# Performance work log

Hardware: AMD Instinct MI355X
Metric: run time of the kernel (lower is better)

## Reference

```python
import jax, jax.numpy as jnp
import numpy as np

B, N, C, K, H, W = 2, 16, 256, 64, 64, 64
NUM_HEADS = 8


def setup_inputs() -> dict:
    key = jax.random.key(0)
    ks = jax.random.split(key, 7)
    return {
        "value": jax.random.normal(ks[0], (B, N, C, H, W), dtype=jnp.float32),
        "key_map": jax.random.normal(ks[1], (B, K, H, W), dtype=jnp.float32),
        "state": jax.random.normal(ks[2], (B, N, K, C), dtype=jnp.float32),
        "b_w": jax.random.normal(ks[3], (NUM_HEADS, C), dtype=jnp.float32) * 0.06,
        "a_w": jax.random.normal(ks[4], (NUM_HEADS, C), dtype=jnp.float32) * 0.06,
        "A_log": jax.random.normal(ks[5], (NUM_HEADS,), dtype=jnp.float32),
        "dt_bias": jax.random.normal(ks[6], (NUM_HEADS,), dtype=jnp.float32),
    }


def reference(value, key_map, state, b_w, a_w, A_log, dt_bias):
    # Gated delta-rule erase-write memory update (state != None branch).
    num_heads = b_w.shape[0]
    rep = value.shape[2] // num_heads  # value_dim // num_heads

    # softmax over key channel dim (stable; matches max-subtract + softmax)
    key_n = jax.nn.softmax(key_map, axis=1)  # [B,K,H,W]

    # v_k = einsum('bkhw, bjhw,bnjv -> bnkv'): fuse via key gram matrix
    # (avoids materializing v_old [B,N,C,H,W])
    gram = jnp.einsum('bkhw,bjhw->bkj', key_n, key_n)      # [B,K,K]
    v_k = jnp.einsum('bkj,bnjv->bnkv', gram, state)        # [B,N,K,C]

    # erase gate beta: sigmoid(state @ b_proj^T), repeat over head groups
    beta = jax.nn.sigmoid(jnp.einsum('bnkc,hc->bnkh', state, b_w))
    beta = jnp.repeat(beta, rep, axis=3)                   # [B,N,K,C]

    # write term
    vk_t = jnp.einsum('bkhw,bnvhw->bnkv', key_n, value)    # [B,N,K,C]

    # decay gate alpha = -exp(A_log) * softplus(state @ a_proj^T + dt_bias)
    alpha = -jnp.exp(A_log) * jax.nn.softplus(
        jnp.einsum('bnkc,hc->bnkh', state, a_w) + dt_bias)
    alpha = jnp.repeat(alpha, rep, axis=3)                 # [B,N,K,C]

    new_state = alpha * (state - beta * v_k) + beta * vk_t  # [B,N,K,C]

    readout = jnp.einsum('bkhw,bnkv->bnvhw', key_n, new_state)  # [B,N,C,H,W]
    return readout
```

## Files before the change

kernel.cpp:

```cpp
#include <hip/hip_runtime.h>
#include <hip/hip_bf16.h>

#define BB 2
#define NN 16
#define CC 256
#define KK 64
#define HW 4096
#define NH 8

typedef __attribute__((ext_vector_type(4))) float f32x4;
typedef __attribute__((ext_vector_type(8))) short s16x8;
typedef __attribute__((ext_vector_type(4))) short s16x4;

__device__ __forceinline__ short f2bf(float f) {
    __hip_bfloat16 h = __float2bfloat16(f);
    return *reinterpret_cast<short*>(&h);
}
__device__ __forceinline__ float bf2f(short s) {
    unsigned int u = ((unsigned int)(unsigned short)s) << 16;
    float f; __builtin_memcpy(&f, &u, 4); return f;
}

__global__ __launch_bounds__(64) void k_softmax(const float* __restrict__ km,
                                                short* __restrict__ kbf,
                                                short* __restrict__ kbfT) {
    const int b = blockIdx.x >> 7;
    const int hw = (blockIdx.x & 127) * 32 + (threadIdx.x & 31);
    const int half = threadIdx.x >> 5;
    const float* p = km + ((size_t)b * KK + half * 32) * HW + hw;
    float x[32];
    float m = -1e30f;
#pragma unroll
    for (int k = 0; k < 32; k++) { x[k] = p[(size_t)k * HW]; m = fmaxf(m, x[k]); }
    m = fmaxf(m, __shfl_xor(m, 32, 64));
    float s = 0.f;
#pragma unroll
    for (int k = 0; k < 32; k++) { x[k] = __expf(x[k] - m); s += x[k]; }
    s += __shfl_xor(s, 32, 64);
    const float inv = 1.f / s;
    short* q2 = kbf + ((size_t)b * KK + half * 32) * HW + hw;
#pragma unroll
    for (int k = 0; k < 32; k++) {
        x[k] *= inv;
        q2[(size_t)k * HW] = f2bf(x[k]);
    }
    short* q3 = kbfT + ((size_t)b * HW + hw) * KK + half * 32;
#pragma unroll
    for (int k8 = 0; k8 < 32; k8 += 8) {
        s16x8 v;
#pragma unroll
        for (int j = 0; j < 8; j++) v[j] = f2bf(x[k8 + j]);
        *(s16x8*)(q3 + k8) = v;
    }
}

__global__ __launch_bounds__(256) void k_gram(const short* __restrict__ kbf,
                                              float* __restrict__ gram) {
    const int tid = threadIdx.x;
    const int id = blockIdx.x;
    const int b = (id >= 2080) ? 1 : 0;
    const int t = id - b * 2080;
    int k = (int)((sqrtf(8.f * (float)t + 1.f) - 1.f) * 0.5f);
    while ((k + 1) * (k + 2) / 2 <= t) k++;
    while (k * (k + 1) / 2 > t) k--;
    const int j = t - k * (k + 1) / 2;

    const short* pa = kbf + ((size_t)b * KK + k) * HW + tid * 16;
    const short* pb = kbf + ((size_t)b * KK + j) * HW + tid * 16;
    const s16x8 a0 = *(const s16x8*)pa, a1 = *(const s16x8*)(pa + 8);
    const s16x8 b0 = *(const s16x8*)pb, b1 = *(const s16x8*)(pb + 8);
    float s = 0.f;
#pragma unroll
    for (int i = 0; i < 8; i++) {
        s = fmaf(bf2f(a0[i]), bf2f(b0[i]), s);
        s = fmaf(bf2f(a1[i]), bf2f(b1[i]), s);
    }
#pragma unroll
    for (int off = 32; off; off >>= 1) s += __shfl_down(s, off, 64);
    __shared__ float red[4];
    if ((tid & 63) == 0) red[tid >> 6] = s;
    __syncthreads();
    if (tid == 0) {
        const float tot = red[0] + red[1] + red[2] + red[3];
        gram[((size_t)b * KK + k) * KK + j] = tot;
        gram[((size_t)b * KK + j) * KK + k] = tot;
    }
}

__global__ __launch_bounds__(256) void k_gates(const float* __restrict__ state,
                                               const float* __restrict__ b_w,
                                               const float* __restrict__ a_w,
                                               const float* __restrict__ A_log,
                                               const float* __restrict__ dt_bias,
                                               float* __restrict__ betaH,
                                               float* __restrict__ alphaH) {
    const int tid = threadIdx.x;
    const int id = blockIdx.x;
    const int k = id & 63;
    const int bn = id >> 6;
    const float s = state[((size_t)bn * KK + k) * CC + tid];

    float pb[NH], pa[NH];
#pragma unroll
    for (int h = 0; h < NH; h++) {
        pb[h] = s * b_w[h * CC + tid];
        pa[h] = s * a_w[h * CC + tid];
    }
#pragma unroll
    for (int off = 32; off; off >>= 1) {
#pragma unroll
        for (int h = 0; h < NH; h++) {
            pb[h] += __shfl_down(pb[h], off, 64);
            pa[h] += __shfl_down(pa[h], off, 64);
        }
    }
    __shared__ float red[4][2 * NH];
    const int wave = tid >> 6, lane = tid & 63;
    if (lane == 0) {
#pragma unroll
        for (int h = 0; h < NH; h++) { red[wave][h] = pb[h]; red[wave][NH + h] = pa[h]; }
    }
    __syncthreads();
    const int h = tid >> 5;
    float braw = 0.f, araw = 0.f;
#pragma unroll
    for (int w = 0; w < 4; w++) { braw += red[w][h]; araw += red[w][NH + h]; }
    if ((tid & 31) == 0) {
        const float beta = 1.f / (1.f + __expf(-braw));
        const float xx = araw + dt_bias[h];
        const float sp = fmaxf(xx, 0.f) + log1pf(__expf(-fabsf(xx)));
        const float alpha = -__expf(A_log[h]) * sp;
        betaH[(size_t)id * NH + h] = beta;
        alphaH[(size_t)id * NH + h] = alpha;
    }
}

__global__ __launch_bounds__(512) void k_vkt_part(const short* __restrict__ kbf,
                                                  const float* __restrict__ value,
                                                  float* __restrict__ pbuf) {
    const int tid = threadIdx.x;
    const int id = blockIdx.x;
    const int hs = id & 7;
    const int bn = id >> 3;
    const int b  = bn >> 4;
    const int w = tid >> 6, lane = tid & 63;
    const int l15 = lane & 15, hi = lane >> 4;
    const int hw0 = hs * 512;

    __shared__ short Bs[2][256 * 64];
    __shared__ short As[2][64 * 64];

    const int sr = tid >> 3;
    const int sj = tid & 7;
    const float* vbase = value + (size_t)bn * CC * HW + hw0;
    const short* abase = kbf + ((size_t)b * KK + sr) * HW + hw0 + sj * 8;

    f32x4 stgB[2][4][2];
    s16x8 stgA[2];

#define LOADREG(set_, t_)                                                      \
    {                                                                          \
        _Pragma("unroll") for (int i = 0; i < 4; i++) {                        \
            const float* p_ = vbase + (size_t)(sr + i * 64) * HW               \
                              + (t_) * 64 + sj * 8;                            \
            stgB[set_][i][0] = *(const f32x4*)p_;                              \
            stgB[set_][i][1] = *(const f32x4*)(p_ + 4);                        \
        }                                                                      \
        stgA[set_] = *(const s16x8*)(abase + (t_) * 64);                       \
    }
#define WRITE_LDS(set_, buf_)                                                  \
    {                                                                          \
        _Pragma("unroll") for (int i = 0; i < 4; i++) {                        \
            const int r_ = sr + i * 64;                                        \
            s16x8 tv_;                                                         \
            _Pragma("unroll") for (int e = 0; e < 4; e++) {                    \
                tv_[e]     = f2bf(stgB[set_][i][0][e]);                        \
                tv_[4 + e] = f2bf(stgB[set_][i][1][e]);                        \
            }                                                                  \
            *(s16x8*)&Bs[buf_][r_ * 64 + ((sj ^ (r_ & 7)) * 8)] = tv_;         \
        }                                                                      \
        *(s16x8*)&As[buf_][sr * 64 + ((sj ^ (sr & 7)) * 8)] = stgA[set_];      \
    }

    f32x4 acc[4][2];
#pragma unroll
    for (int m = 0; m < 4; m++)
#pragma unroll
        for (int n = 0; n < 2; n++) acc[m][n] = (f32x4){0.f, 0.f, 0.f, 0.f};

    LOADREG(0, 0);
    LOADREG(1, 1);
    WRITE_LDS(0, 0);
    asm volatile("s_waitcnt lgkmcnt(0)" ::: "memory");
    __builtin_amdgcn_s_barrier();

#pragma unroll
    for (int t = 0; t < 8; t++) {
        const int buf = t & 1;
        if (t + 2 < 8) LOADREG(buf, t + 2);

        const int swz = l15 & 7;
#pragma unroll
        for (int s = 0; s < 2; s++) {
            s16x8 bfr[2];
#pragma unroll
            for (int n = 0; n < 2; n++)
                bfr[n] = *(const s16x8*)&Bs[buf][(w * 32 + n * 16 + l15) * 64 +
                                                (((s * 4 + hi) ^ swz) * 8)];
#pragma unroll
            for (int m = 0; m < 4; m++) {
                const s16x8 afr = *(const s16x8*)&As[buf][(m * 16 + l15) * 64 +
                                                          (((s * 4 + hi) ^ swz) * 8)];
                acc[m][0] = __builtin_amdgcn_mfma_f32_16x16x32_bf16(afr, bfr[0],
                                                                    acc[m][0], 0, 0, 0);
                acc[m][1] = __builtin_amdgcn_mfma_f32_16x16x32_bf16(afr, bfr[1],
                                                                    acc[m][1], 0, 0, 0);
            }
        }
        asm volatile("s_waitcnt lgkmcnt(0)" ::: "memory");
        __builtin_amdgcn_s_barrier();
        if (t + 1 < 8) {
            WRITE_LDS((t + 1) & 1, (t + 1) & 1);
            asm volatile("s_waitcnt lgkmcnt(0)" ::: "memory");
            __builtin_amdgcn_s_barrier();
        }
    }
#undef LOADREG
#undef WRITE_LDS

    float* op = pbuf + (size_t)id * (KK * CC);
#pragma unroll
    for (int m = 0; m < 4; m++)
#pragma unroll
        for (int n = 0; n < 2; n++)
#pragma unroll
            for (int r = 0; r < 4; r++)
                op[(m * 16 + hi * 4 + r) * CC + w * 32 + n * 16 + l15] = acc[m][n][r];
}

__global__ __launch_bounds__(256) void k_combine(const float* __restrict__ pbuf,
                                                 const float* __restrict__ gram,
                                                 const float* __restrict__ state,
                                                 const float* __restrict__ betaH,
                                                 const float* __restrict__ alphaH,
                                                 short* __restrict__ nsT) {
    const int tid = threadIdx.x;
    const int id = blockIdx.x;
    const int ct = id & 15;
    const int bn = id >> 4;
    const int b  = bn >> 4;
    const int head = ct >> 1;

    __shared__ float gramL[KK][65];
    __shared__ float stL[KK][17];
    __shared__ float alphaL[KK], betaL[KK];
    __shared__ float nsb[KK][17];

    for (int i = tid; i < KK * KK; i += 256)
        gramL[i >> 6][i & 63] = gram[(size_t)b * KK * KK + i];
    for (int i = tid; i < KK * 16; i += 256)
        stL[i >> 4][i & 15] = state[((size_t)bn * KK + (i >> 4)) * CC + ct * 16 + (i & 15)];
    if (tid < KK) {
        alphaL[tid] = alphaH[((size_t)bn * KK + tid) * NH + head];
        betaL[tid]  = betaH[((size_t)bn * KK + tid) * NH + head];
    }
    __syncthreads();

    const int k = tid >> 2, cq = (tid & 3) * 4;

    f32x4 vkt = (f32x4){0.f, 0.f, 0.f, 0.f};
#pragma unroll
    for (int hs = 0; hs < 8; hs++) {
        const f32x4 p = *(const f32x4*)(pbuf + ((size_t)(bn * 8 + hs) * KK + k) * CC +
                                        ct * 16 + cq);
        vkt += p;
    }

    float vk[4] = {0.f, 0.f, 0.f, 0.f};
#pragma unroll 8
    for (int j = 0; j < KK; j++) {
        const float g = gramL[k][j];
        vk[0] = fmaf(g, stL[j][cq + 0], vk[0]);
        vk[1] = fmaf(g, stL[j][cq + 1], vk[1]);
        vk[2] = fmaf(g, stL[j][cq + 2], vk[2]);
        vk[3] = fmaf(g, stL[j][cq + 3], vk[3]);
    }
    const float al = alphaL[k], be = betaL[k];
#pragma unroll
    for (int i = 0; i < 4; i++)
        nsb[k][cq + i] = al * (stL[k][cq + i] - be * vk[i]) + be * vkt[i];
    __syncthreads();

    const int c = tid >> 4, k4 = (tid & 15) * 4;
    s16x4 v;
#pragma unroll
    for (int i = 0; i < 4; i++) v[i] = f2bf(nsb[k4 + i][c]);
    *(s16x4*)(nsT + ((size_t)bn * CC + ct * 16 + c) * KK + k4) = v;
}

__global__ __launch_bounds__(256) void k_readout_mfma(const short* __restrict__ kbfT,
                                                      const short* __restrict__ nsT,
                                                      float* __restrict__ out) {
    const int tid = threadIdx.x;
    const int id = blockIdx.x;
    const int hwt = id & 63;
    const int bn  = id >> 6;
    const int b   = bn >> 4;
    const int w = tid >> 6, lane = tid & 63;
    const int l15 = lane & 15, hi = lane >> 4;
    const int hw0 = hwt * 64 + w * 16;

    const short* Bp = kbfT + ((size_t)b * HW + hw0 + l15) * KK + hi * 8;
    const s16x8 b0 = *(const s16x8*)Bp;
    const s16x8 b1 = *(const s16x8*)(Bp + 32);

    const short* Ap = nsT + ((size_t)bn * CC + l15) * KK + hi * 8;
    float* op = out + ((size_t)bn * CC + hi * 4) * HW + hw0 + l15;

#pragma unroll
    for (int ct = 0; ct < 16; ct++) {
        const s16x8 a0 = *(const s16x8*)(Ap + (size_t)(ct * 16) * KK);
        const s16x8 a1 = *(const s16x8*)(Ap + (size_t)(ct * 16) * KK + 32);
        f32x4 acc = (f32x4){0.f, 0.f, 0.f, 0.f};
        acc = __builtin_amdgcn_mfma_f32_16x16x32_bf16(a0, b0, acc, 0, 0, 0);
        acc = __builtin_amdgcn_mfma_f32_16x16x32_bf16(a1, b1, acc, 0, 0, 0);
#pragma unroll
        for (int r = 0; r < 4; r++)
            op[(size_t)(ct * 16 + r) * HW] = acc[r];
    }
}

extern "C" void kernel_launch(void* const* d_in, const int* in_sizes, int n_in,
                              void* d_out, int out_size, void* d_ws, size_t ws_size,
                              hipStream_t stream) {
    const float* value   = (const float*)d_in[0];
    const float* key_map = (const float*)d_in[1];
    const float* state   = (const float*)d_in[2];
    const float* b_w     = (const float*)d_in[3];
    const float* a_w     = (const float*)d_in[4];
    const float* A_log   = (const float*)d_in[5];
    const float* dt_bias = (const float*)d_in[6];
    float* out = (float*)d_out;

    short* kbf   = (short*)d_ws;
    short* kbfT  = kbf + 524288;
    float* gram  = (float*)(kbfT + 524288);
    float* betaH = gram + 8192;
    float* alphaH= betaH + 16384;
    short* nsT   = (short*)(alphaH + 16384);
    float* pbuf  = (float*)(nsT + 524288);

    k_softmax<<<BB * (HW / 32), 64, 0, stream>>>(key_map, kbf, kbfT);
    k_gram<<<BB * (KK * (KK + 1) / 2), 256, 0, stream>>>(kbf, gram);
    k_gates<<<BB * NN * KK, 256, 0, stream>>>(state, b_w, a_w, A_log, dt_bias,
                                              betaH, alphaH);
    k_vkt_part<<<BB * NN * 8, 512, 0, stream>>>(kbf, value, pbuf);
    k_combine<<<BB * NN * 16, 256, 0, stream>>>(pbuf, gram, state, betaH, alphaH, nsT);
    k_readout_mfma<<<BB * NN * (HW / 64), 256, 0, stream>>>(kbfT, nsT, out);
}
```

Before: 103.5 us.

## Merge softmax and gate kernels; swap MFMA operands for vectorized stores

```diff
diff --git a/kernel.cpp b/kernel.cpp
--- a/kernel.cpp
+++ b/kernel.cpp
@@ -21,36 +21,89 @@
     float f; __builtin_memcpy(&f, &u, 4); return f;
 }
 
-__global__ __launch_bounds__(64) void k_softmax(const float* __restrict__ km,
-                                                short* __restrict__ kbf,
-                                                short* __restrict__ kbfT) {
-    const int b = blockIdx.x >> 7;
-    const int hw = (blockIdx.x & 127) * 32 + (threadIdx.x & 31);
-    const int half = threadIdx.x >> 5;
-    const float* p = km + ((size_t)b * KK + half * 32) * HW + hw;
-    float x[32];
-    float m = -1e30f;
-#pragma unroll
-    for (int k = 0; k < 32; k++) { x[k] = p[(size_t)k * HW]; m = fmaxf(m, x[k]); }
-    m = fmaxf(m, __shfl_xor(m, 32, 64));
-    float s = 0.f;
-#pragma unroll
-    for (int k = 0; k < 32; k++) { x[k] = __expf(x[k] - m); s += x[k]; }
-    s += __shfl_xor(s, 32, 64);
-    const float inv = 1.f / s;
-    short* q2 = kbf + ((size_t)b * KK + half * 32) * HW + hw;
-#pragma unroll
-    for (int k = 0; k < 32; k++) {
-        x[k] *= inv;
-        q2[(size_t)k * HW] = f2bf(x[k]);
-    }
-    short* q3 = kbfT + ((size_t)b * HW + hw) * KK + half * 32;
-#pragma unroll
-    for (int k8 = 0; k8 < 32; k8 += 8) {
-        s16x8 v;
-#pragma unroll
-        for (int j = 0; j < 8; j++) v[j] = f2bf(x[k8 + j]);
-        *(s16x8*)(q3 + k8) = v;
+__global__ __launch_bounds__(256) void k_pre(const float* __restrict__ state,
+                                             const float* __restrict__ b_w,
+                                             const float* __restrict__ a_w,
+                                             const float* __restrict__ A_log,
+                                             const float* __restrict__ dt_bias,
+                                             float* __restrict__ betaH,
+                                             float* __restrict__ alphaH,
+                                             const float* __restrict__ km,
+                                             short* __restrict__ kbf,
+                                             short* __restrict__ kbfT) {
+    __shared__ float red[4][2 * NH];
+    const int tid = threadIdx.x;
+    const int bid = blockIdx.x;
+
+    if (bid < BB * NN * KK) {
+        const int id = bid;
+        const int bn = id >> 6;
+        const int k = id & 63;
+        const float s = state[((size_t)bn * KK + k) * CC + tid];
+
+        float pb[NH], pa[NH];
+#pragma unroll
+        for (int h = 0; h < NH; h++) {
+            pb[h] = s * b_w[h * CC + tid];
+            pa[h] = s * a_w[h * CC + tid];
+        }
+#pragma unroll
+        for (int off = 32; off; off >>= 1) {
+#pragma unroll
+            for (int h = 0; h < NH; h++) {
+                pb[h] += __shfl_down(pb[h], off, 64);
+                pa[h] += __shfl_down(pa[h], off, 64);
+            }
+        }
+        const int wave = tid >> 6, lane = tid & 63;
+        if (lane == 0) {
+#pragma unroll
+            for (int h = 0; h < NH; h++) { red[wave][h] = pb[h]; red[wave][NH + h] = pa[h]; }
+        }
+        __syncthreads();
+        const int h = tid >> 5;
+        float braw = 0.f, araw = 0.f;
+#pragma unroll
+        for (int w = 0; w < 4; w++) { braw += red[w][h]; araw += red[w][NH + h]; }
+        if ((tid & 31) == 0) {
+            const float beta = 1.f / (1.f + __expf(-braw));
+            const float xx = araw + dt_bias[h];
+            const float sp = fmaxf(xx, 0.f) + log1pf(__expf(-fabsf(xx)));
+            const float alpha = -__expf(A_log[h]) * sp;
+            betaH[(size_t)id * NH + h] = beta;
+            alphaH[(size_t)id * NH + h] = alpha;
+        }
+    } else {
+        const int sid = bid - BB * NN * KK;
+        const int b = sid >> 5;
+        const int w = tid >> 6, lane = tid & 63;
+        const int hw = (sid & 31) * 128 + w * 32 + (lane & 31);
+        const int half = lane >> 5;
+        const float* p = km + ((size_t)b * KK + half * 32) * HW + hw;
+        float x[32];
+        float m = -1e30f;
+#pragma unroll
+        for (int k = 0; k < 32; k++) { x[k] = p[(size_t)k * HW]; m = fmaxf(m, x[k]); }
+        m = fmaxf(m, __shfl_xor(m, 32, 64));
+        float s = 0.f;
+#pragma unroll
+        for (int k = 0; k < 32; k++) { x[k] = __expf(x[k] - m); s += x[k]; }
+        s += __shfl_xor(s, 32, 64);
+        const float inv = 1.f / s;
+        short* q2 = kbf + ((size_t)b * KK + half * 32) * HW + hw;
+#pragma unroll
+        for (int k = 0; k < 32; k++) {
+            x[k] *= inv;
+            q2[(size_t)k * HW] = f2bf(x[k]);
+        }
+        short* q3 = kbfT + ((size_t)b * HW + hw) * KK + half * 32;
+#pragma unroll
+        for (int k8 = 0; k8 < 32; k8 += 8) {
+            s16x8 v;
+#pragma unroll
+            for (int j = 0; j < 8; j++) v[j] = f2bf(x[k8 + j]);
+            *(s16x8*)(q3 + k8) = v;
+        }
     }
 }
 
@@ -84,54 +137,6 @@
         const float tot = red[0] + red[1] + red[2] + red[3];
         gram[((size_t)b * KK + k) * KK + j] = tot;
         gram[((size_t)b * KK + j) * KK + k] = tot;
-    }
-}
-
-__global__ __launch_bounds__(256) void k_gates(const float* __restrict__ state,
-                                               const float* __restrict__ b_w,
-                                               const float* __restrict__ a_w,
-                                               const float* __restrict__ A_log,
-                                               const float* __restrict__ dt_bias,
-                                               float* __restrict__ betaH,
-                                               float* __restrict__ alphaH) {
-    const int tid = threadIdx.x;
-    const int id = blockIdx.x;
-    const int k = id & 63;
-    const int bn = id >> 6;
-    const float s = state[((size_t)bn * KK + k) * CC + tid];
-
-    float pb[NH], pa[NH];
-#pragma unroll
-    for (int h = 0; h < NH; h++) {
-        pb[h] = s * b_w[h * CC + tid];
-        pa[h] = s * a_w[h * CC + tid];
-    }
-#pragma unroll
-    for (int off = 32; off; off >>= 1) {
-#pragma unroll
-        for (int h = 0; h < NH; h++) {
-            pb[h] += __shfl_down(pb[h], off, 64);
-            pa[h] += __shfl_down(pa[h], off, 64);
-        }
-    }
-    __shared__ float red[4][2 * NH];
-    const int wave = tid >> 6, lane = tid & 63;
-    if (lane == 0) {
-#pragma unroll
-        for (int h = 0; h < NH; h++) { red[wave][h] = pb[h]; red[wave][NH + h] = pa[h]; }
-    }
-    __syncthreads();
-    const int h = tid >> 5;
-    float braw = 0.f, araw = 0.f;
-#pragma unroll
-    for (int w = 0; w < 4; w++) { braw += red[w][h]; araw += red[w][NH + h]; }
-    if ((tid & 31) == 0) {
-        const float beta = 1.f / (1.f + __expf(-braw));
-        const float xx = araw + dt_bias[h];
-        const float sp = fmaxf(xx, 0.f) + log1pf(__expf(-fabsf(xx)));
-        const float alpha = -__expf(A_log[h]) * sp;
-        betaH[(size_t)id * NH + h] = beta;
-        alphaH[(size_t)id * NH + h] = alpha;
     }
 }
 
@@ -182,11 +187,11 @@
         *(s16x8*)&As[buf_][sr * 64 + ((sj ^ (sr & 7)) * 8)] = stgA[set_];      \
     }
 
-    f32x4 acc[4][2];
-#pragma unroll
-    for (int m = 0; m < 4; m++)
-#pragma unroll
-        for (int n = 0; n < 2; n++) acc[m][n] = (f32x4){0.f, 0.f, 0.f, 0.f};
+    f32x4 acc[2][4];
+#pragma unroll
+    for (int m2 = 0; m2 < 2; m2++)
+#pragma unroll
+        for (int n4 = 0; n4 < 4; n4++) acc[m2][n4] = (f32x4){0.f, 0.f, 0.f, 0.f};
 
     LOADREG(0, 0);
     LOADREG(1, 1);
@@ -202,19 +207,19 @@
         const int swz = l15 & 7;
 #pragma unroll
         for (int s = 0; s < 2; s++) {
-            s16x8 bfr[2];
-#pragma unroll
-            for (int n = 0; n < 2; n++)
-                bfr[n] = *(const s16x8*)&Bs[buf][(w * 32 + n * 16 + l15) * 64 +
-                                                (((s * 4 + hi) ^ swz) * 8)];
-#pragma unroll
-            for (int m = 0; m < 4; m++) {
-                const s16x8 afr = *(const s16x8*)&As[buf][(m * 16 + l15) * 64 +
+            s16x8 vfr[2];
+#pragma unroll
+            for (int m2 = 0; m2 < 2; m2++)
+                vfr[m2] = *(const s16x8*)&Bs[buf][(w * 32 + m2 * 16 + l15) * 64 +
+                                                 (((s * 4 + hi) ^ swz) * 8)];
+#pragma unroll
+            for (int n4 = 0; n4 < 4; n4++) {
+                const s16x8 afr = *(const s16x8*)&As[buf][(n4 * 16 + l15) * 64 +
                                                           (((s * 4 + hi) ^ swz) * 8)];
-                acc[m][0] = __builtin_amdgcn_mfma_f32_16x16x32_bf16(afr, bfr[0],
-                                                                    acc[m][0], 0, 0, 0);
-                acc[m][1] = __builtin_amdgcn_mfma_f32_16x16x32_bf16(afr, bfr[1],
-                                                                    acc[m][1], 0, 0, 0);
+                acc[0][n4] = __builtin_amdgcn_mfma_f32_16x16x32_bf16(vfr[0], afr,
+                                                                     acc[0][n4], 0, 0, 0);
+                acc[1][n4] = __builtin_amdgcn_mfma_f32_16x16x32_bf16(vfr[1], afr,
+                                                                     acc[1][n4], 0, 0, 0);
             }
         }
         asm volatile("s_waitcnt lgkmcnt(0)" ::: "memory");
@@ -230,12 +235,13 @@
 
     float* op = pbuf + (size_t)id * (KK * CC);
 #pragma unroll
-    for (int m = 0; m < 4; m++)
-#pragma unroll
-        for (int n = 0; n < 2; n++)
-#pragma unroll
-            for (int r = 0; r < 4; r++)
-                op[(m * 16 + hi * 4 + r) * CC + w * 32 + n * 16 + l15] = acc[m][n][r];
+    for (int m2 = 0; m2 < 2; m2++)
+#pragma unroll
+        for (int n4 = 0; n4 < 4; n4++) {
+            const int k = n4 * 16 + l15;
+            const int c = w * 32 + m2 * 16 + hi * 4;
+            *(f32x4*)(op + k * CC + c) = acc[m2][n4];
+        }
 }
 
 __global__ __launch_bounds__(256) void k_combine(const float* __restrict__ pbuf,
@@ -311,22 +317,20 @@
     const int hw0 = hwt * 64 + w * 16;
 
     const short* Bp = kbfT + ((size_t)b * HW + hw0 + l15) * KK + hi * 8;
-    const s16x8 b0 = *(const s16x8*)Bp;
-    const s16x8 b1 = *(const s16x8*)(Bp + 32);
+    const s16x8 hwf0 = *(const s16x8*)Bp;
+    const s16x8 hwf1 = *(const s16x8*)(Bp + 32);
 
     const short* Ap = nsT + ((size_t)bn * CC + l15) * KK + hi * 8;
-    float* op = out + ((size_t)bn * CC + hi * 4) * HW + hw0 + l15;
+    float* op = out + ((size_t)bn * CC + l15) * HW + hw0 + hi * 4;
 
 #pragma unroll
     for (int ct = 0; ct < 16; ct++) {
         const s16x8 a0 = *(const s16x8*)(Ap + (size_t)(ct * 16) * KK);
         const s16x8 a1 = *(const s16x8*)(Ap + (size_t)(ct * 16) * KK + 32);
         f32x4 acc = (f32x4){0.f, 0.f, 0.f, 0.f};
-        acc = __builtin_amdgcn_mfma_f32_16x16x32_bf16(a0, b0, acc, 0, 0, 0);
-        acc = __builtin_amdgcn_mfma_f32_16x16x32_bf16(a1, b1, acc, 0, 0, 0);
-#pragma unroll
-        for (int r = 0; r < 4; r++)
-            op[(size_t)(ct * 16 + r) * HW] = acc[r];
+        acc = __builtin_amdgcn_mfma_f32_16x16x32_bf16(hwf0, a0, acc, 0, 0, 0);
+        acc = __builtin_amdgcn_mfma_f32_16x16x32_bf16(hwf1, a1, acc, 0, 0, 0);
+        *(f32x4*)(op + (size_t)(ct * 16) * HW) = acc;
     }
 }
 
@@ -350,10 +354,9 @@
     short* nsT   = (short*)(alphaH + 16384);
     float* pbuf  = (float*)(nsT + 524288);
 
-    k_softmax<<<BB * (HW / 32), 64, 0, stream>>>(key_map, kbf, kbfT);
+    k_pre<<<BB * NN * KK + BB * (HW / 128), 256, 0, stream>>>(
+        state, b_w, a_w, A_log, dt_bias, betaH, alphaH, key_map, kbf, kbfT);
     k_gram<<<BB * (KK * (KK + 1) / 2), 256, 0, stream>>>(kbf, gram);
-    k_gates<<<BB * NN * KK, 256, 0, stream>>>(state, b_w, a_w, A_log, dt_bias,
-                                              betaH, alphaH);
     k_vkt_part<<<BB * NN * 8, 512, 0, stream>>>(kbf, value, pbuf);
     k_combine<<<BB * NN * 16, 256, 0, stream>>>(pbuf, gram, state, betaH, alphaH, nsT);
     k_readout_mfma<<<BB * NN * (HW / 64), 256, 0, stream>>>(kbfT, nsT, out);
```

After: 104.9 us. No clear change (+1.4%).
